# Performance work log

Measured on AMD Instinct MI355X. Metric: run time of the kernel, lower is better.

The kernel has to match this reference:

```python
import jax, jax.numpy as jnp
import numpy as np
import math

N_HEADS = 16
FACTOR = 5


def setup_inputs() -> dict:
    key = jax.random.key(0)
    ks = jax.random.split(key, 9)
    B, T, D = 2, 2048, 1024
    s = D ** -0.5
    return {
        "x": jax.random.normal(ks[0], (B, T, D), dtype=jnp.float32),
        "Wq": jax.random.normal(ks[1], (D, D), dtype=jnp.float32) * s,
        "bq": jnp.zeros((D,), dtype=jnp.float32),
        "Wk": jax.random.normal(ks[2], (D, D), dtype=jnp.float32) * s,
        "bk": jnp.zeros((D,), dtype=jnp.float32),
        "Wv": jax.random.normal(ks[3], (D, D), dtype=jnp.float32) * s,
        "bv": jnp.zeros((D,), dtype=jnp.float32),
        "Wo": jax.random.normal(ks[4], (D, D), dtype=jnp.float32) * s,
        "bo": jnp.zeros((D,), dtype=jnp.float32),
    }


def reference(x, Wq, bq, Wk, bk, Wv, bv, Wo, bo):
    B, T, D = x.shape
    H = N_HEADS
    Hd = D // H
    scale = Hd ** -0.5

    def proj(W, b):
        # [B,T,D] -> [B,H,T,Hd]
        return (x @ W + b).reshape(B, T, H, Hd).transpose(0, 2, 1, 3)

    q = proj(Wq, bq)
    k = proj(Wk, bk)
    v = proj(Wv, bv)

    # ProbSparse query selection: top-u queries by L1 norm per (b,h)
    q_norm = jnp.sum(jnp.abs(q), axis=-1)              # [B,H,T]
    u = min(int(FACTOR * math.log(T)), T)              # static (38 for T=2048)
    _, index = jax.lax.top_k(q_norm, u)                # [B,H,u]

    # Dense causal scores (matches original module's math)
    scores = jnp.einsum('bhqd,bhkd->bhqk', q, k) * scale   # [B,H,T,T]
    causal = jnp.tril(jnp.ones((T, T), dtype=bool))
    scores = jnp.where(causal, scores, -jnp.inf)

    # Gather selected query rows, softmax, weighted sum of V (vectorized over B,H)
    sel_scores = jnp.take_along_axis(scores, index[..., None], axis=2)  # [B,H,u,T]
    sel_attn = jax.nn.softmax(sel_scores, axis=-1)
    sel_out = jnp.einsum('bhut,bhtd->bhud', sel_attn, v)                # [B,H,u,Hd]

    # Scatter back into zeros at selected query positions (indices are unique)
    attn_output = jnp.zeros_like(q)
    bI = jnp.arange(B)[:, None, None]
    hI = jnp.arange(H)[None, :, None]
    attn_output = attn_output.at[bI, hI, index].set(sel_out)

    out = attn_output.transpose(0, 2, 1, 3).reshape(B, T, D)
    return out @ Wo + bo
```

## Files before the change

kernel.cpp:

```cpp
#include <hip/hip_runtime.h>

#define NB 2
#define T_SEQ 2048
#define D_MODEL 1024
#define NH 16
#define HD 64
#define U_SEL 38
#define CAND_CAP 96
#define NCH 8

typedef __attribute__((ext_vector_type(8))) short s16x8;
typedef __attribute__((ext_vector_type(4))) short s16x4;
typedef __attribute__((ext_vector_type(4))) float f32x4;
typedef unsigned short ushort_t;

__device__ __forceinline__ unsigned short f2bf(float f) {
    unsigned u = __float_as_uint(f);
    u += 0x7FFFu + ((u >> 16) & 1u);
    return (unsigned short)(u >> 16);
}
__device__ __forceinline__ float bf2f(unsigned short h) {
    return __uint_as_float(((unsigned)h) << 16);
}

__device__ __forceinline__ void async_copy16(const void* g, void* l) {
    __builtin_amdgcn_global_load_lds(
        (const __attribute__((address_space(1))) void*)g,
        (__attribute__((address_space(3))) void*)l, 16, 0, 0);
}

__global__ __launch_bounds__(256) void prep(
    const float* __restrict__ x,
    const float* __restrict__ Wq, const float* __restrict__ Wk, const float* __restrict__ Wv,
    ushort_t* __restrict__ xh,
    ushort_t* __restrict__ wqhT, ushort_t* __restrict__ wkhT, ushort_t* __restrict__ wvhT)
{
    __shared__ float T[64][68];
    const int tid = threadIdx.x;
    if (blockIdx.x < 2048) {
        const size_t i0 = ((size_t)blockIdx.x * 256 + tid) * 8;
        const f32x4 a = *(const f32x4*)(x + i0);
        const f32x4 b = *(const f32x4*)(x + i0 + 4);
        const float f[8] = {a.x, a.y, a.z, a.w, b.x, b.y, b.z, b.w};
        s16x8 hi;
        #pragma unroll
        for (int e = 0; e < 8; ++e) hi[e] = (short)f2bf(f[e]);
        *(s16x8*)(xh + i0) = hi;
        return;
    }
    const int id2 = blockIdx.x - 2048;
    const int z = id2 >> 8;
    const int rem = id2 & 255;
    const int k0 = (rem & 15) * 64, n0 = (rem >> 4) * 64;
    const float* W = (z == 0) ? Wq : (z == 1) ? Wk : Wv;

    #pragma unroll
    for (int i = 0; i < 4; ++i) {
        const int r = (tid >> 4) + i * 16, c = (tid & 15) * 4;
        *(f32x4*)&T[r][c] = *(const f32x4*)&W[(size_t)(k0 + r) * D_MODEL + n0 + c];
    }
    __syncthreads();

    const int n = tid >> 2, kq = (tid & 3) * 16;
    s16x8 hi0, hi1;
    #pragma unroll
    for (int j = 0; j < 16; ++j) {
        const float f = T[kq + j][n];
        if (j < 8) hi0[j] = (short)f2bf(f);
        else       hi1[j - 8] = (short)f2bf(f);
    }
    ushort_t* oh = (z == 0) ? wqhT : (z == 1) ? wkhT : wvhT;
    const size_t ob = (size_t)(n0 + n) * D_MODEL + k0 + kq;
    *(s16x8*)(oh + ob) = hi0;
    *(s16x8*)(oh + ob + 8) = hi1;
}

#define GBM 128
#define GBN 128
#define GBK 32

__global__ __launch_bounds__(256, 4) void qkv_mfma(
    const ushort_t* __restrict__ xh,
    const ushort_t* __restrict__ wqhT, const ushort_t* __restrict__ wkhT,
    const ushort_t* __restrict__ wvhT,
    const float* __restrict__ bq, const float* __restrict__ bk, const float* __restrict__ bv,
    ushort_t* __restrict__ qb, ushort_t* __restrict__ ko, ushort_t* __restrict__ vT,
    float* __restrict__ norms)
{
    const int z = blockIdx.z;
    __shared__ ushort_t Ah[GBM * GBK];
    __shared__ ushort_t Bh[GBN * GBK];

    const int tid = threadIdx.x;
    const int lane = tid & 63;
    const int wid = tid >> 6;
    const int wr = wid >> 1, wc = wid & 1;
    const size_t rowBase = (size_t)blockIdx.x * GBM;
    const size_t colBase = (size_t)blockIdx.y * GBN;

    const ushort_t* B0 = (z == 0) ? wqhT : (z == 1) ? wkhT : wvhT;
    const int srow = tid >> 2;
    const int sl0  = ((tid & 3) - (srow >> 1)) & 3;
    const int skq  = sl0 * 8;

    const ushort_t* pA0 = xh + (rowBase + srow) * D_MODEL + skq;
    const ushort_t* pA1 = pA0 + (size_t)64 * D_MODEL;
    const ushort_t* pB0 = B0 + (colBase + srow) * D_MODEL + skq;
    const ushort_t* pB1 = pB0 + (size_t)64 * D_MODEL;
    ushort_t* lA0 = &Ah[tid * 8];
    ushort_t* lA1 = &Ah[2048 + tid * 8];
    ushort_t* lB0 = &Bh[tid * 8];
    ushort_t* lB1 = &Bh[2048 + tid * 8];

    int aph[4], bph[4];
    #pragma unroll
    for (int i = 0; i < 4; ++i) {
        const int arow = wr * 64 + i * 16 + (lane & 15);
        aph[i] = arow * GBK + ((((lane >> 4) + (arow >> 1)) & 3) << 3);
        const int brow = wc * 64 + i * 16 + (lane & 15);
        bph[i] = brow * GBK + ((((lane >> 4) + (brow >> 1)) & 3) << 3);
    }

    f32x4 acc[4][4] = {};

    for (int kk = 0; kk < 32; ++kk) {
        async_copy16(pA0, lA0);
        async_copy16(pA1, lA1);
        async_copy16(pB0, lB0);
        async_copy16(pB1, lB1);
        pA0 += GBK; pA1 += GBK; pB0 += GBK; pB1 += GBK;
        __syncthreads();

        s16x8 bf[4];
        #pragma unroll
        for (int j = 0; j < 4; ++j) bf[j] = *(const s16x8*)&Bh[bph[j]];
        #pragma unroll
        for (int i = 0; i < 4; ++i) {
            const s16x8 af = *(const s16x8*)&Ah[aph[i]];
            #pragma unroll
            for (int j = 0; j < 4; ++j)
                acc[i][j] = __builtin_amdgcn_mfma_f32_16x16x32_bf16(af, bf[j], acc[i][j], 0, 0, 0);
        }
        __syncthreads();
    }

    const int cB = (int)colBase + wc * 64 + (lane & 15);
    const int rL = wr * 64 + ((lane >> 4) << 2);
    const int rB = (int)rowBase + rL;
    if (z == 0) {
        float bjv[4];
        #pragma unroll
        for (int j = 0; j < 4; ++j) bjv[j] = bq[cB + j * 16];
        const int bb = (int)(rowBase >> 11);
        const int hw = cB >> 6;
        #pragma unroll
        for (int i = 0; i < 4; ++i) {
            float nr[4];
            #pragma unroll
            for (int r = 0; r < 4; ++r) {
                float s = 0.f;
                #pragma unroll
                for (int j = 0; j < 4; ++j) s += fabsf(acc[i][j][r] + bjv[j]);
                nr[r] = s;
            }
            #pragma unroll
            for (int off = 1; off < 16; off <<= 1) {
                #pragma unroll
                for (int r = 0; r < 4; ++r) nr[r] += __shfl_xor(nr[r], off);
            }
            if ((lane & 15) == 0) {
                const int trow = (int)(rowBase & (T_SEQ - 1)) + wr * 64 + i * 16 + ((lane >> 4) << 2);
                f32x4 nv; nv.x = nr[0]; nv.y = nr[1]; nv.z = nr[2]; nv.w = nr[3];
                *(f32x4*)&norms[(size_t)(bb * NH + hw) * T_SEQ + trow] = nv;
            }
        }
        #pragma unroll
        for (int j = 0; j < 4; ++j)
            #pragma unroll
            for (int i = 0; i < 4; ++i)
                #pragma unroll
                for (int r = 0; r < 4; ++r)
                    qb[(size_t)(rB + i * 16 + r) * D_MODEL + cB + j * 16] = f2bf(acc[i][j][r] + bjv[j]);
    } else if (z == 1) {
        #pragma unroll
        for (int j = 0; j < 4; ++j) {
            const float bj = bk[cB + j * 16];
            #pragma unroll
            for (int i = 0; i < 4; ++i)
                #pragma unroll
                for (int r = 0; r < 4; ++r)
                    ko[(size_t)(rB + i * 16 + r) * D_MODEL + cB + j * 16] = f2bf(acc[i][j][r] + bj);
        }
    } else {
        const int bb = (int)(rowBase >> 11);
        const int tBase = (int)(rowBase & (T_SEQ - 1)) + rL;
        #pragma unroll
        for (int j = 0; j < 4; ++j) {
            const int dg = cB + j * 16;
            const float bj = bv[dg];
            ushort_t* vrow = vT + ((size_t)(bb * NH) * HD + dg) * T_SEQ;
            #pragma unroll
            for (int i = 0; i < 4; ++i) {
                s16x4 pk;
                #pragma unroll
                for (int r = 0; r < 4; ++r)
                    pk[r] = (short)f2bf(acc[i][j][r] + bj);
                *(s16x4*)&vrow[tBase + i * 16] = pk;
            }
        }
    }
}

__global__ __launch_bounds__(256) void topk_select(
    const float* __restrict__ norms, int* __restrict__ cand_t, int* __restrict__ cand_cnt,
    unsigned* __restrict__ selmask)
{
    const int bh = blockIdx.x;
    const int tid = threadIdx.x;
    const int lane = tid & 63;
    const int w = tid >> 6;

    if (tid < 128) selmask[bh * 128 + tid] = 0u;

    __shared__ unsigned keys[T_SEQ];
    __shared__ unsigned hist[2048];
    __shared__ unsigned wsum[4];
    __shared__ unsigned bc_bin, bc_above;
    __shared__ int cnt;

    const float* nr = norms + (size_t)bh * T_SEQ;
    #pragma unroll
    for (int j = 0; j < 8; ++j)
        keys[tid + j * 256] = __float_as_uint(nr[tid + j * 256]);

    const int  shifts[3] = {21, 10, 0};
    const unsigned binm[3]  = {0x7FFu, 0x7FFu, 0x3FFu};
    const unsigned prefm[3] = {0x00000000u, 0xFFE00000u, 0xFFFFFC00u};

    unsigned prefix = 0;
    unsigned K_rem = U_SEL;

    for (int p = 0; p < 3; ++p) {
        #pragma unroll
        for (int j = 0; j < 8; ++j) hist[tid + j * 256] = 0;
        __syncthreads();
        #pragma unroll
        for (int j = 0; j < 8; ++j) {
            const unsigned k = keys[tid + j * 256];
            if ((k & prefm[p]) == prefix)
                atomicAdd(&hist[(k >> shifts[p]) & binm[p]], 1u);
        }
        __syncthreads();

        unsigned s = 0;
        #pragma unroll
        for (int e = 0; e < 8; ++e) s += hist[tid * 8 + e];
        unsigned v = s;
        #pragma unroll
        for (int off = 1; off < 64; off <<= 1) {
            const unsigned o = __shfl_down((int)v, off);
            if (lane + off < 64) v += o;
        }
        if (lane == 0) wsum[w] = v;
        __syncthreads();
        unsigned suf = v;
        for (int ww = w + 1; ww < 4; ++ww) suf += wsum[ww];
        const unsigned suf_next = suf - s;

        if (suf >= K_rem && suf_next < K_rem) {
            unsigned acc = suf_next;
            #pragma unroll
            for (int e = 7; e >= 0; --e) {
                const unsigned nb = hist[tid * 8 + e];
                if (acc + nb >= K_rem) { bc_bin = tid * 8 + e; bc_above = acc; break; }
                acc += nb;
            }
        }
        __syncthreads();
        prefix |= bc_bin << shifts[p];
        K_rem -= bc_above;
        __syncthreads();
    }

    const float thr = __uint_as_float(prefix) - 0.4f;
    if (tid == 0) cnt = 0;
    __syncthreads();
    #pragma unroll
    for (int j = 0; j < 8; ++j) {
        const int i = tid + j * 256;
        if (__uint_as_float(keys[i]) >= thr) {
            const int s = atomicAdd(&cnt, 1);
            if (s < CAND_CAP) cand_t[bh * CAND_CAP + s] = i;
        }
    }
    __syncthreads();
    if (tid == 0) cand_cnt[bh] = cnt < CAND_CAP ? cnt : CAND_CAP;
}

__global__ __launch_bounds__(256) void fixup_norms(
    const float* __restrict__ x, const float* __restrict__ Wq,
    const float* __restrict__ bq, const int* __restrict__ cand_t,
    const int* __restrict__ cand_cnt, float* __restrict__ n_exact)
{
    const int bh = blockIdx.x, c = blockIdx.y;
    const int b = bh >> 4, h = bh & 15;
    if (c >= cand_cnt[bh]) return;
    const int t = cand_t[bh * CAND_CAP + c];
    const int tid = threadIdx.x, d = tid & 63, kq = tid >> 6;

    __shared__ float xs[D_MODEL];
    __shared__ float part[4][HD];

    *(f32x4*)&xs[tid * 4] = *(const f32x4*)&x[((size_t)(b * T_SEQ + t)) * D_MODEL + tid * 4];
    __syncthreads();

    const float* wp = Wq + (size_t)(kq * 256) * D_MODEL + h * HD + d;
    const float* xp = &xs[kq * 256];
    float a0 = 0.f, a1 = 0.f, a2 = 0.f, a3 = 0.f;
    #pragma unroll 4
    for (int k = 0; k < 256; k += 4) {
        a0 += xp[k]     * wp[(k)     * D_MODEL];
        a1 += xp[k + 1] * wp[(k + 1) * D_MODEL];
        a2 += xp[k + 2] * wp[(k + 2) * D_MODEL];
        a3 += xp[k + 3] * wp[(k + 3) * D_MODEL];
    }
    part[kq][d] = (a0 + a1) + (a2 + a3);
    __syncthreads();
    if (tid < 64) {
        float v = fabsf(part[0][tid] + part[1][tid] + part[2][tid] + part[3][tid]
                        + bq[h * HD + tid]);
        #pragma unroll
        for (int off = 1; off < 64; off <<= 1) v += __shfl_xor(v, off);
        if (tid == 0) n_exact[bh * CAND_CAP + c] = v;
    }
}

__global__ __launch_bounds__(128) void fixup_select(
    const float* __restrict__ n_exact, const int* __restrict__ cand_t,
    const int* __restrict__ cand_cnt, int* __restrict__ idx_out,
    unsigned* __restrict__ selmask, int* __restrict__ selu)
{
    const int bh = blockIdx.x;
    const int tid = threadIdx.x;
    const int nc = cand_cnt[bh];
    const int b = bh >> 4, h = bh & 15;

    __shared__ float nv[CAND_CAP];
    __shared__ int   tv[CAND_CAP];

    if (tid < nc) {
        nv[tid] = n_exact[bh * CAND_CAP + tid];
        tv[tid] = cand_t[bh * CAND_CAP + tid];
    }
    __syncthreads();

    if (tid < nc) {
        const float ni = nv[tid];
        const int   ti = tv[tid];
        int rank = 0;
        for (int j = 0; j < nc; ++j) {
            const float njv = nv[j];
            const int   tj  = tv[j];
            rank += (njv > ni || (njv == ni && tj < ti)) ? 1 : 0;
        }
        if (rank < U_SEL) {
            idx_out[bh * U_SEL + rank] = ti;
            const int row = (b << 11) + ti;
            atomicOr(&selmask[row], 1u << h);
            selu[row * NH + h] = rank;
        }
    }
}

__global__ __launch_bounds__(256) void attn_scores(
    const ushort_t* __restrict__ qb, const ushort_t* __restrict__ kk_,
    const int* __restrict__ idx, float* __restrict__ S,
    float* __restrict__ mstat, float* __restrict__ lstat)
{
    const int bh = blockIdx.x, ch = blockIdx.y, ug = blockIdx.z;
    const int b = bh >> 4, h = bh & 15;
    const int tid = threadIdx.x;
    const int lane = tid & 63;
    const int w = tid >> 6;
    const int t = ch * 256 + tid;
    const int u0 = ug * 19;

    __shared__ float qs[19][HD];
    __shared__ int qis[19];
    __shared__ float mpart[19][4];
    __shared__ float lpart[19][4];

    if (tid < 19) qis[tid] = idx[bh * U_SEL + u0 + tid];
    if (tid < 76) { mpart[tid >> 2][tid & 3] = -1e30f; lpart[tid >> 2][tid & 3] = 0.f; }
    __syncthreads();
    for (int e = tid; e < 19 * HD; e += 256) {
        const int u = e >> 6, d = e & 63;
        qs[u][d] = bf2f(qb[((size_t)(b * T_SEQ + qis[u])) * D_MODEL + h * HD + d]) * 0.125f;
    }

    float kr[64];
    {
        const ushort_t* kp = kk_ + ((size_t)(b * T_SEQ + t)) * D_MODEL + h * HD;
        #pragma unroll
        for (int d0 = 0; d0 < 64; d0 += 8) {
            const s16x8 r = *(const s16x8*)(kp + d0);
            #pragma unroll
            for (int e = 0; e < 8; ++e) kr[d0 + e] = bf2f((unsigned short)r[e]);
        }
    }
    __syncthreads();

    const int wbase = ch * 256 + (tid & ~63);
    for (int uu = 0; uu < 19; ++uu) {
        const int qi = qis[uu];
        if (wbase > qi) continue;
        float sp0 = 0.f, sp1 = 0.f, sp2 = 0.f, sp3 = 0.f;
        #pragma unroll
        for (int d0 = 0; d0 < 64; d0 += 16) {
            const f32x4 q0 = *(const f32x4*)&qs[uu][d0];
            const f32x4 q1 = *(const f32x4*)&qs[uu][d0 + 4];
            const f32x4 q2 = *(const f32x4*)&qs[uu][d0 + 8];
            const f32x4 q3 = *(const f32x4*)&qs[uu][d0 + 12];
            sp0 += q0.x * kr[d0] + q0.y * kr[d0 + 1] + q0.z * kr[d0 + 2] + q0.w * kr[d0 + 3];
            sp1 += q1.x * kr[d0 + 4] + q1.y * kr[d0 + 5] + q1.z * kr[d0 + 6] + q1.w * kr[d0 + 7];
            sp2 += q2.x * kr[d0 + 8] + q2.y * kr[d0 + 9] + q2.z * kr[d0 + 10] + q2.w * kr[d0 + 11];
            sp3 += q3.x * kr[d0 + 12] + q3.y * kr[d0 + 13] + q3.z * kr[d0 + 14] + q3.w * kr[d0 + 15];
        }
        const float s = sp0 + sp1 + sp2 + sp3;
        S[((size_t)(bh * U_SEL + u0 + uu)) * T_SEQ + t] = s;
        const float sm = (t <= qi) ? s : -1e30f;
        float mw = sm;
        #pragma unroll
        for (int off = 1; off < 64; off <<= 1) mw = fmaxf(mw, __shfl_xor(mw, off));
        float p = (t <= qi) ? __expf(s - mw) : 0.f;
        #pragma unroll
        for (int off = 1; off < 64; off <<= 1) p += __shfl_xor(p, off);
        if (lane == 0) { mpart[uu][w] = mw; lpart[uu][w] = p; }
    }
    __syncthreads();
    if (tid < 19) {
        float M = -1e30f;
        #pragma unroll
        for (int ww = 0; ww < 4; ++ww) M = fmaxf(M, mpart[tid][ww]);
        float L = 0.f;
        #pragma unroll
        for (int ww = 0; ww < 4; ++ww) {
            const float mw = mpart[tid][ww];
            if (mw > -1e29f) L += lpart[tid][ww] * __expf(mw - M);
        }
        const size_t si = (size_t)(bh * U_SEL + u0 + tid) * NCH + ch;
        mstat[si] = M;
        lstat[si] = L;
    }
}

__global__ __launch_bounds__(256) void attn_pv(
    const float* __restrict__ S, const ushort_t* __restrict__ vT,
    const int* __restrict__ idx, const float* __restrict__ mstat,
    const float* __restrict__ lstat, float* __restrict__ sel_out)
{
    const int bh = blockIdx.x, u = blockIdx.y;
    const int tid = threadIdx.x;
    const int d = tid & 63;
    const int qtr = tid >> 6;
    const int qi = idx[bh * U_SEL + u];
    const int nk = qi + 1;
    const int pad8 = (nk + 7) & ~7;
    const float* Srow = S + ((size_t)(bh * U_SEL + u)) * T_SEQ;

    __shared__ float sc[T_SEQ];
    __shared__ float part[4][HD];

    const float* mp = mstat + (size_t)(bh * U_SEL + u) * NCH;
    const float* lp = lstat + (size_t)(bh * U_SEL + u) * NCH;
    float M = -1e30f;
    #pragma unroll
    for (int c = 0; c < NCH; ++c) M = fmaxf(M, mp[c]);
    float L = 0.f;
    #pragma unroll
    for (int c = 0; c < NCH; ++c) {
        const float mc = mp[c];
        if (mc > -1e29f) L += lp[c] * __expf(mc - M);
    }

    for (int t = tid; t < nk; t += 256) sc[t] = __expf(Srow[t] - M);
    if (tid < 7) { const int t = nk + tid; if (t < pad8) sc[t] = 0.f; }
    __syncthreads();

    const ushort_t* vrow = vT + ((size_t)(bh * HD + d)) * T_SEQ;
    float a0 = 0.f, a1 = 0.f;
    #pragma unroll
    for (int mm = 0; mm < 4; ++mm) {
        const int base = mm * 512 + qtr * 128;
        if (base >= nk) break;
        const int bend = base + 128 < pad8 ? base + 128 : pad8;
        for (int t = base; t < bend; t += 8) {
            const s16x8 v8 = *(const s16x8*)(vrow + t);
            const f32x4 p0 = *(const f32x4*)&sc[t];
            const f32x4 p1 = *(const f32x4*)&sc[t + 4];
            a0 += p0.x * bf2f((unsigned short)v8[0]) + p0.y * bf2f((unsigned short)v8[1])
                + p0.z * bf2f((unsigned short)v8[2]) + p0.w * bf2f((unsigned short)v8[3]);
            a1 += p1.x * bf2f((unsigned short)v8[4]) + p1.y * bf2f((unsigned short)v8[5])
                + p1.z * bf2f((unsigned short)v8[6]) + p1.w * bf2f((unsigned short)v8[7]);
        }
    }
    part[qtr][d] = a0 + a1;
    __syncthreads();
    if (tid < HD)
        sel_out[((size_t)(bh * U_SEL + u)) * HD + tid] =
            (part[0][tid] + part[1][tid] + part[2][tid] + part[3][tid]) / L;
}

__global__ __launch_bounds__(256) void out_proj(
    const float* __restrict__ sel_out, const float* __restrict__ Wo,
    const float* __restrict__ bo, const unsigned* __restrict__ selmask,
    const int* __restrict__ selu, float* __restrict__ out)
{
    const int row = blockIdx.x;
    const int b = row >> 11;
    const int tid = threadIdx.x;
    const int c0 = tid * 4;

    __shared__ float s[HD];
    f32x4 o = *(const f32x4*)&bo[c0];
    unsigned mask = selmask[row];

    while (mask) {
        const int h = __ffs(mask) - 1;
        mask &= mask - 1;
        const int u = selu[row * NH + h];
        if (tid < HD)
            s[tid] = sel_out[((size_t)((b * NH + h) * U_SEL + u)) * HD + tid];
        __syncthreads();
        #pragma unroll 8
        for (int r = 0; r < HD; ++r) {
            const float sv = s[r];
            const f32x4 w4 = *(const f32x4*)&Wo[((size_t)(h * HD + r)) * D_MODEL + c0];
            o.x += sv * w4.x; o.y += sv * w4.y; o.z += sv * w4.z; o.w += sv * w4.w;
        }
        __syncthreads();
    }
    *(f32x4*)&out[(size_t)row * D_MODEL + c0] = o;
}

extern "C" void kernel_launch(void* const* d_in, const int* in_sizes, int n_in,
                              void* d_out, int out_size, void* d_ws, size_t ws_size,
                              hipStream_t stream)
{
    const float* x  = (const float*)d_in[0];
    const float* Wq = (const float*)d_in[1];
    const float* bq = (const float*)d_in[2];
    const float* Wk = (const float*)d_in[3];
    const float* bk = (const float*)d_in[4];
    const float* Wv = (const float*)d_in[5];
    const float* bv = (const float*)d_in[6];
    const float* Wo = (const float*)d_in[7];
    const float* bo = (const float*)d_in[8];
    float* out = (float*)d_out;

    char* ws = (char*)d_ws;
    ushort_t* xh      = (ushort_t*)(ws);
    ushort_t* wqhT    = (ushort_t*)(ws + (8u << 20));
    ushort_t* wkhT    = (ushort_t*)(ws + (10u << 20));
    ushort_t* wvhT    = (ushort_t*)(ws + (12u << 20));
    ushort_t* k       = (ushort_t*)(ws + (14u << 20));
    ushort_t* vT      = (ushort_t*)(ws + (22u << 20));
    ushort_t* qb      = (ushort_t*)(ws + (30u << 20));
    float*    S       = (float*)(ws + (38u << 20));
    float*    norms   = (float*)(ws + (48u << 20));
    int*      cand_t  = (int*)(ws + (48u << 20) + (256u << 10));
    int*      cand_cnt= (int*)(ws + (48u << 20) + (272u << 10));
    float*    n_exact = (float*)(ws + (48u << 20) + (276u << 10));
    int*      idx     = (int*)(ws + (48u << 20) + (292u << 10));
    float*    sel_out = (float*)(ws + (48u << 20) + (300u << 10));
    unsigned* selmask = (unsigned*)(ws + (48u << 20) + (640u << 10));
    int*      selu    = (int*)(ws + (48u << 20) + (656u << 10));
    float*    mstat   = (float*)(ws + (48u << 20) + (912u << 10));
    float*    lstat   = (float*)(ws + (48u << 20) + (960u << 10));

    prep<<<2048 + 768, 256, 0, stream>>>(x, Wq, Wk, Wv, xh, wqhT, wkhT, wvhT);
    {
        dim3 g((NB * T_SEQ) / GBM, D_MODEL / GBN, 3);
        qkv_mfma<<<g, 256, 0, stream>>>(xh, wqhT, wkhT, wvhT, bq, bk, bv,
                                        qb, k, vT, norms);
    }
    topk_select<<<NB * NH, 256, 0, stream>>>(norms, cand_t, cand_cnt, selmask);
    {
        dim3 g(NB * NH, CAND_CAP);
        fixup_norms<<<g, 256, 0, stream>>>(x, Wq, bq, cand_t, cand_cnt, n_exact);
    }
    fixup_select<<<NB * NH, 128, 0, stream>>>(n_exact, cand_t, cand_cnt, idx, selmask, selu);
    {
        dim3 g(NB * NH, T_SEQ / 256, 2);
        attn_scores<<<g, 256, 0, stream>>>(qb, k, idx, S, mstat, lstat);
    }
    {
        dim3 g(NB * NH, U_SEL);
        attn_pv<<<g, 256, 0, stream>>>(S, vT, idx, mstat, lstat, sel_out);
    }
    out_proj<<<NB * T_SEQ, 256, 0, stream>>>(sel_out, Wo, bo, selmask, selu, out);
}
```

Before: 161.8 us.

## Drop bf16 Q store; use exact fixup Q rows and rework PV reduction

The QKV GEMM no longer writes the full bf16 Q tensor. The fixup kernel now saves the exact fp32 query vectors for candidates, and a rank-to-candidate map lets attn_scores read them directly. attn_pv is rewritten so each wave handles 16 head dims, with lanes striding over time and a shuffle reduction at the end, removing the shared-memory staging and syncs. This saves large scattered global stores at the cost of more cross-lane reductions.

```diff
diff --git a/kernel.cpp b/kernel.cpp
--- a/kernel.cpp
+++ b/kernel.cpp
@@ -84,7 +84,7 @@
     const ushort_t* __restrict__ wqhT, const ushort_t* __restrict__ wkhT,
     const ushort_t* __restrict__ wvhT,
     const float* __restrict__ bq, const float* __restrict__ bk, const float* __restrict__ bv,
-    ushort_t* __restrict__ qb, ushort_t* __restrict__ ko, ushort_t* __restrict__ vT,
+    ushort_t* __restrict__ ko, ushort_t* __restrict__ vT,
     float* __restrict__ norms)
 {
     const int z = blockIdx.z;
@@ -174,13 +174,6 @@
                 *(f32x4*)&norms[(size_t)(bb * NH + hw) * T_SEQ + trow] = nv;
             }
         }
-        #pragma unroll
-        for (int j = 0; j < 4; ++j)
-            #pragma unroll
-            for (int i = 0; i < 4; ++i)
-                #pragma unroll
-                for (int r = 0; r < 4; ++r)
-                    qb[(size_t)(rB + i * 16 + r) * D_MODEL + cB + j * 16] = f2bf(acc[i][j][r] + bjv[j]);
     } else if (z == 1) {
         #pragma unroll
         for (int j = 0; j < 4; ++j) {
@@ -300,7 +293,8 @@
 __global__ __launch_bounds__(256) void fixup_norms(
     const float* __restrict__ x, const float* __restrict__ Wq,
     const float* __restrict__ bq, const int* __restrict__ cand_t,
-    const int* __restrict__ cand_cnt, float* __restrict__ n_exact)
+    const int* __restrict__ cand_cnt, float* __restrict__ n_exact,
+    float* __restrict__ q_exact)
 {
     const int bh = blockIdx.x, c = blockIdx.y;
     const int b = bh >> 4, h = bh & 15;
@@ -327,8 +321,10 @@
     part[kq][d] = (a0 + a1) + (a2 + a3);
     __syncthreads();
     if (tid < 64) {
-        float v = fabsf(part[0][tid] + part[1][tid] + part[2][tid] + part[3][tid]
-                        + bq[h * HD + tid]);
+        const float qd = part[0][tid] + part[1][tid] + part[2][tid] + part[3][tid]
+                       + bq[h * HD + tid];
+        q_exact[((size_t)(bh * CAND_CAP + c)) * HD + tid] = qd;
+        float v = fabsf(qd);
         #pragma unroll
         for (int off = 1; off < 64; off <<= 1) v += __shfl_xor(v, off);
         if (tid == 0) n_exact[bh * CAND_CAP + c] = v;
@@ -338,7 +334,8 @@
 __global__ __launch_bounds__(128) void fixup_select(
     const float* __restrict__ n_exact, const int* __restrict__ cand_t,
     const int* __restrict__ cand_cnt, int* __restrict__ idx_out,
-    unsigned* __restrict__ selmask, int* __restrict__ selu)
+    unsigned* __restrict__ selmask, int* __restrict__ selu,
+    int* __restrict__ rank2c)
 {
     const int bh = blockIdx.x;
     const int tid = threadIdx.x;
@@ -365,6 +362,7 @@
         }
         if (rank < U_SEL) {
             idx_out[bh * U_SEL + rank] = ti;
+            rank2c[bh * U_SEL + rank] = tid;
             const int row = (b << 11) + ti;
             atomicOr(&selmask[row], 1u << h);
             selu[row * NH + h] = rank;
@@ -373,9 +371,9 @@
 }
 
 __global__ __launch_bounds__(256) void attn_scores(
-    const ushort_t* __restrict__ qb, const ushort_t* __restrict__ kk_,
-    const int* __restrict__ idx, float* __restrict__ S,
-    float* __restrict__ mstat, float* __restrict__ lstat)
+    const float* __restrict__ q_exact, const int* __restrict__ rank2c,
+    const ushort_t* __restrict__ kk_, const int* __restrict__ idx,
+    float* __restrict__ S, float* __restrict__ mstat, float* __restrict__ lstat)
 {
     const int bh = blockIdx.x, ch = blockIdx.y, ug = blockIdx.z;
     const int b = bh >> 4, h = bh & 15;
@@ -387,15 +385,19 @@
 
     __shared__ float qs[19][HD];
     __shared__ int qis[19];
+    __shared__ int qcs[19];
     __shared__ float mpart[19][4];
     __shared__ float lpart[19][4];
 
-    if (tid < 19) qis[tid] = idx[bh * U_SEL + u0 + tid];
+    if (tid < 19) {
+        qis[tid] = idx[bh * U_SEL + u0 + tid];
+        qcs[tid] = rank2c[bh * U_SEL + u0 + tid];
+    }
     if (tid < 76) { mpart[tid >> 2][tid & 3] = -1e30f; lpart[tid >> 2][tid & 3] = 0.f; }
     __syncthreads();
     for (int e = tid; e < 19 * HD; e += 256) {
         const int u = e >> 6, d = e & 63;
-        qs[u][d] = bf2f(qb[((size_t)(b * T_SEQ + qis[u])) * D_MODEL + h * HD + d]) * 0.125f;
+        qs[u][d] = q_exact[((size_t)(bh * CAND_CAP + qcs[u])) * HD + d] * 0.125f;
     }
 
     float kr[64];
@@ -461,15 +463,11 @@
 {
     const int bh = blockIdx.x, u = blockIdx.y;
     const int tid = threadIdx.x;
-    const int d = tid & 63;
-    const int qtr = tid >> 6;
+    const int lane = tid & 63;
+    const int w = tid >> 6;
     const int qi = idx[bh * U_SEL + u];
     const int nk = qi + 1;
-    const int pad8 = (nk + 7) & ~7;
     const float* Srow = S + ((size_t)(bh * U_SEL + u)) * T_SEQ;
-
-    __shared__ float sc[T_SEQ];
-    __shared__ float part[4][HD];
 
     const float* mp = mstat + (size_t)(bh * U_SEL + u) * NCH;
     const float* lp = lstat + (size_t)(bh * U_SEL + u) * NCH;
@@ -483,32 +481,41 @@
         if (mc > -1e29f) L += lp[c] * __expf(mc - M);
     }
 
-    for (int t = tid; t < nk; t += 256) sc[t] = __expf(Srow[t] - M);
-    if (tid < 7) { const int t = nk + tid; if (t < pad8) sc[t] = 0.f; }
-    __syncthreads();
-
-    const ushort_t* vrow = vT + ((size_t)(bh * HD + d)) * T_SEQ;
-    float a0 = 0.f, a1 = 0.f;
-    #pragma unroll
-    for (int mm = 0; mm < 4; ++mm) {
-        const int base = mm * 512 + qtr * 128;
-        if (base >= nk) break;
-        const int bend = base + 128 < pad8 ? base + 128 : pad8;
-        for (int t = base; t < bend; t += 8) {
-            const s16x8 v8 = *(const s16x8*)(vrow + t);
-            const f32x4 p0 = *(const f32x4*)&sc[t];
-            const f32x4 p1 = *(const f32x4*)&sc[t + 4];
-            a0 += p0.x * bf2f((unsigned short)v8[0]) + p0.y * bf2f((unsigned short)v8[1])
-                + p0.z * bf2f((unsigned short)v8[2]) + p0.w * bf2f((unsigned short)v8[3]);
-            a1 += p1.x * bf2f((unsigned short)v8[4]) + p1.y * bf2f((unsigned short)v8[5])
-                + p1.z * bf2f((unsigned short)v8[6]) + p1.w * bf2f((unsigned short)v8[7]);
-        }
-    }
-    part[qtr][d] = a0 + a1;
-    __syncthreads();
-    if (tid < HD)
-        sel_out[((size_t)(bh * U_SEL + u)) * HD + tid] =
-            (part[0][tid] + part[1][tid] + part[2][tid] + part[3][tid]) / L;
+    float acc[16] = {};
+    const ushort_t* vbase = vT + ((size_t)(bh * HD + w * 16)) * T_SEQ;
+
+    for (int tb = 0; tb < nk; tb += 512) {
+        const int t0 = tb + lane * 8;
+        const f32x4 s0 = *(const f32x4*)(Srow + t0);
+        const f32x4 s1 = *(const f32x4*)(Srow + t0 + 4);
+        float p[8];
+        p[0] = (t0 + 0 < nk) ? __expf(s0.x - M) : 0.f;
+        p[1] = (t0 + 1 < nk) ? __expf(s0.y - M) : 0.f;
+        p[2] = (t0 + 2 < nk) ? __expf(s0.z - M) : 0.f;
+        p[3] = (t0 + 3 < nk) ? __expf(s0.w - M) : 0.f;
+        p[4] = (t0 + 4 < nk) ? __expf(s1.x - M) : 0.f;
+        p[5] = (t0 + 5 < nk) ? __expf(s1.y - M) : 0.f;
+        p[6] = (t0 + 6 < nk) ? __expf(s1.z - M) : 0.f;
+        p[7] = (t0 + 7 < nk) ? __expf(s1.w - M) : 0.f;
+
+        #pragma unroll
+        for (int dd = 0; dd < 16; ++dd) {
+            const s16x8 v8 = *(const s16x8*)(vbase + (size_t)dd * T_SEQ + t0);
+            acc[dd] += p[0] * bf2f((unsigned short)v8[0]) + p[1] * bf2f((unsigned short)v8[1])
+                     + p[2] * bf2f((unsigned short)v8[2]) + p[3] * bf2f((unsigned short)v8[3])
+                     + p[4] * bf2f((unsigned short)v8[4]) + p[5] * bf2f((unsigned short)v8[5])
+                     + p[6] * bf2f((unsigned short)v8[6]) + p[7] * bf2f((unsigned short)v8[7]);
+        }
+    }
+
+    float* orow = sel_out + ((size_t)(bh * U_SEL + u)) * HD + w * 16;
+    #pragma unroll
+    for (int dd = 0; dd < 16; ++dd) {
+        float v = acc[dd];
+        #pragma unroll
+        for (int off = 1; off < 64; off <<= 1) v += __shfl_xor(v, off);
+        if (lane == 0) orow[dd] = v / L;
+    }
 }
 
 __global__ __launch_bounds__(256) void out_proj(
@@ -565,7 +572,6 @@
     ushort_t* wvhT    = (ushort_t*)(ws + (12u << 20));
     ushort_t* k       = (ushort_t*)(ws + (14u << 20));
     ushort_t* vT      = (ushort_t*)(ws + (22u << 20));
-    ushort_t* qb      = (ushort_t*)(ws + (30u << 20));
     float*    S       = (float*)(ws + (38u << 20));
     float*    norms   = (float*)(ws + (48u << 20));
     int*      cand_t  = (int*)(ws + (48u << 20) + (256u << 10));
@@ -577,22 +583,25 @@
     int*      selu    = (int*)(ws + (48u << 20) + (656u << 10));
     float*    mstat   = (float*)(ws + (48u << 20) + (912u << 10));
     float*    lstat   = (float*)(ws + (48u << 20) + (960u << 10));
+    float*    q_exact = (float*)(ws + (49u << 20));
+    int*      rank2c  = (int*)(ws + (49u << 20) + (800u << 10));
 
     prep<<<2048 + 768, 256, 0, stream>>>(x, Wq, Wk, Wv, xh, wqhT, wkhT, wvhT);
     {
         dim3 g((NB * T_SEQ) / GBM, D_MODEL / GBN, 3);
         qkv_mfma<<<g, 256, 0, stream>>>(xh, wqhT, wkhT, wvhT, bq, bk, bv,
-                                        qb, k, vT, norms);
+                                        k, vT, norms);
     }
     topk_select<<<NB * NH, 256, 0, stream>>>(norms, cand_t, cand_cnt, selmask);
     {
         dim3 g(NB * NH, CAND_CAP);
-        fixup_norms<<<g, 256, 0, stream>>>(x, Wq, bq, cand_t, cand_cnt, n_exact);
-    }
-    fixup_select<<<NB * NH, 128, 0, stream>>>(n_exact, cand_t, cand_cnt, idx, selmask, selu);
+        fixup_norms<<<g, 256, 0, stream>>>(x, Wq, bq, cand_t, cand_cnt, n_exact, q_exact);
+    }
+    fixup_select<<<NB * NH, 128, 0, stream>>>(n_exact, cand_t, cand_cnt, idx,
+                                              selmask, selu, rank2c);
     {
         dim3 g(NB * NH, T_SEQ / 256, 2);
-        attn_scores<<<g, 256, 0, stream>>>(qb, k, idx, S, mstat, lstat);
+        attn_scores<<<g, 256, 0, stream>>>(q_exact, rank2c, k, idx, S, mstat, lstat);
     }
     {
         dim3 g(NB * NH, U_SEL);
```

Result: faster. 150.7 us (-6.9%).
